# Kernel optimization log

Hardware: AMD Instinct MI355X
Metric: run time of the kernel (lower is better)

The kernel has to match this reference:

```python
import jax, jax.numpy as jnp
from jax import lax
import numpy as np

B, H, W, C = 64, 224, 224, 3
OH, OW = 224, 224
EPS = 1e-3  # keras BatchNormalization default epsilon
FLAT = 52 * 52 * 10  # after conv7(valid)->pool2->conv5(valid)->pool2 on 224x224


def setup_inputs() -> dict:
    key = jax.random.key(0)
    ks = jax.random.split(key, 6)
    return {
        "x": jax.random.normal(ks[0], (B, H, W, C), jnp.float32),
        "c1_w": jax.random.normal(ks[1], (7, 7, C, 8), jnp.float32) * 0.05,
        "c1_b": jnp.zeros((8,), jnp.float32),
        "g1": jnp.ones((8,), jnp.float32),
        "b1": jnp.zeros((8,), jnp.float32),
        "m1": jnp.zeros((8,), jnp.float32),
        "v1": jnp.ones((8,), jnp.float32),
        "c2_w": jax.random.normal(ks[2], (5, 5, 8, 10), jnp.float32) * 0.05,
        "c2_b": jnp.zeros((10,), jnp.float32),
        "g2": jnp.ones((10,), jnp.float32),
        "b2": jnp.zeros((10,), jnp.float32),
        "m2": jnp.zeros((10,), jnp.float32),
        "v2": jnp.ones((10,), jnp.float32),
        "d1_w": jax.random.normal(ks[3], (FLAT, 32), jnp.float32) * 0.01,
        "d1_b": jnp.zeros((32,), jnp.float32),
        "d2_w": jax.random.normal(ks[4], (32, 6), jnp.float32) * 0.01,
        "d2_b": jnp.array([1.0, 0.0, 0.0, 0.0, 1.0, 0.0], jnp.float32),  # identity affine
    }


def _conv(x, w, b):
    return lax.conv_general_dilated(x, w, (1, 1), 'VALID',
                                    dimension_numbers=('NHWC', 'HWIO', 'NHWC')) + b


def _maxpool(x):
    return lax.reduce_window(x, -jnp.inf, lax.max, (1, 2, 2, 1), (1, 2, 2, 1), 'VALID')


def _bn(x, g, b, m, v):
    # inference-mode batchnorm: gamma*(x-mean)/sqrt(var+eps)+beta
    return (x - m) * lax.rsqrt(v + EPS) * g + b


def _bilinear(img, px, py):
    # img: [H,W,C]; px,py: [OH,OW] pixel-space sample coords; zero fill outside
    x0 = jnp.floor(px).astype(jnp.int32)
    y0 = jnp.floor(py).astype(jnp.int32)

    def gather(yi, xi):
        valid = (yi >= 0) & (yi < H) & (xi >= 0) & (xi < W)
        v = img[jnp.clip(yi, 0, H - 1), jnp.clip(xi, 0, W - 1)]  # [OH,OW,C]
        return v * valid[..., None]

    wx = (px - x0)[..., None]
    wy = (py - y0)[..., None]
    return (gather(y0, x0) * (1 - wx) * (1 - wy)
            + gather(y0, x0 + 1) * wx * (1 - wy)
            + gather(y0 + 1, x0) * (1 - wx) * wy
            + gather(y0 + 1, x0 + 1) * wx * wy)


def reference(x, c1_w, c1_b, g1, b1, m1, v1, c2_w, c2_b, g2, b2, m2, v2,
              d1_w, d1_b, d2_w, d2_b):
    # localization network
    h = _maxpool(_bn(jax.nn.relu(_conv(x, c1_w, c1_b)), g1, b1, m1, v1))
    h = _maxpool(_bn(jax.nn.relu(_conv(h, c2_w, c2_b)), g2, b2, m2, v2))
    h = h.reshape(h.shape[0], -1)                      # [B, FLAT]
    h = jax.nn.relu(h @ d1_w + d1_b)                   # [B, 32]
    theta = (h @ d2_w + d2_b).reshape(-1, 2, 3)        # [B, 2, 3]

    # normalized homogeneous grid [N,3] with N = OH*OW
    xs = jnp.linspace(-1.0, 1.0, OW)
    ys = jnp.linspace(-1.0, 1.0, OH)
    xg, yg = jnp.meshgrid(xs, ys)
    grid = jnp.stack([xg.ravel(), yg.ravel(), jnp.ones(OH * OW, jnp.float32)], axis=-1)

    coords = jnp.einsum('bij,nj->bni', theta, grid)    # [B, N, 2]
    px = ((coords[..., 0] + 1.0) * 0.5 * (W - 1)).reshape(-1, OH, OW)
    py = ((coords[..., 1] + 1.0) * 0.5 * (H - 1)).reshape(-1, OH, OW)
    return jax.vmap(_bilinear)(x, px, py)              # [B, OH, OW, C]
```

## Files before the change

### kernel.cpp

```cpp
#include <hip/hip_runtime.h>
#include <hip/hip_bf16.h>


#define NCHUNK 212
#define KC 128

__global__ __launch_bounds__(256) void k_conv1(
    const float* __restrict__ x, const float* __restrict__ w,
    const float* __restrict__ bias, const float* __restrict__ g,
    const float* __restrict__ bt, const float* __restrict__ m,
    const float* __restrict__ v, float* __restrict__ out) {
  __shared__ float s_in[3][38][40];
  __shared__ float s_scale[8], s_shift[8], s_bias[8];
  const int tid = threadIdx.x;
  const int bx = blockIdx.x, by = blockIdx.y, b = blockIdx.z;

  if (tid < 8) {
    float sc = g[tid] * rsqrtf(v[tid] + 1e-3f);
    s_scale[tid] = sc;
    s_shift[tid] = bt[tid] - m[tid] * sc;
    s_bias[tid] = bias[tid];
  }
  const int iy0 = by * 32, ix0 = bx * 32;
  const float* xb = x + (size_t)b * 224 * 224 * 3;
  for (int f = tid; f < 38 * 114; f += 256) {
    int r = f / 114, rem = f - r * 114;
    int q = rem / 3, c = rem - q * 3;
    int gy = iy0 + r; if (gy > 223) gy = 223;
    int gc = ix0 + q; if (gc > 223) gc = 223;
    s_in[c][r][q] = xb[(gy * 224 + gc) * 3 + c];
  }
  __syncthreads();

  const int pyl = tid >> 4, pxl = tid & 15;
  const int ly = 2 * pyl, lx = 2 * pxl;
  float acc[4][8];
#pragma unroll
  for (int i = 0; i < 4; i++)
#pragma unroll
    for (int j = 0; j < 8; j++) acc[i][j] = 0.f;

#pragma unroll 1
  for (int r = 0; r < 8; ++r) {
    float row[3][8];
#pragma unroll
    for (int ci = 0; ci < 3; ci++)
#pragma unroll
      for (int j = 0; j < 4; j++) {
        float2 t = *(const float2*)&s_in[ci][ly + r][lx + 2 * j];
        row[ci][2 * j] = t.x; row[ci][2 * j + 1] = t.y;
      }
    if (r < 7) {
#pragma unroll
      for (int kx = 0; kx < 7; kx++)
#pragma unroll
        for (int ci = 0; ci < 3; ci++) {
          const float* wp = &w[((r * 7 + kx) * 3 + ci) * 8];
          float i0 = row[ci][kx], i1 = row[ci][kx + 1];
#pragma unroll
          for (int co = 0; co < 8; co++) {
            float wv = wp[co];
            acc[0][co] = fmaf(i0, wv, acc[0][co]);
            acc[1][co] = fmaf(i1, wv, acc[1][co]);
          }
        }
    }
    if (r >= 1) {
#pragma unroll
      for (int kx = 0; kx < 7; kx++)
#pragma unroll
        for (int ci = 0; ci < 3; ci++) {
          const float* wp = &w[(((r - 1) * 7 + kx) * 3 + ci) * 8];
          float i0 = row[ci][kx], i1 = row[ci][kx + 1];
#pragma unroll
          for (int co = 0; co < 8; co++) {
            float wv = wp[co];
            acc[2][co] = fmaf(i0, wv, acc[2][co]);
            acc[3][co] = fmaf(i1, wv, acc[3][co]);
          }
        }
    }
  }

  const int py = by * 16 + pyl, px = bx * 16 + pxl;
  if (py < 109 && px < 109) {
#pragma unroll
    for (int co = 0; co < 8; co++) {
      float sc = s_scale[co], sh = s_shift[co], bs = s_bias[co];
      float a0 = fmaxf(acc[0][co] + bs, 0.f) * sc + sh;
      float a1 = fmaxf(acc[1][co] + bs, 0.f) * sc + sh;
      float a2 = fmaxf(acc[2][co] + bs, 0.f) * sc + sh;
      float a3 = fmaxf(acc[3][co] + bs, 0.f) * sc + sh;
      out[(((size_t)co * 64 + b) * 109 + py) * 109 + px] =
          fmaxf(fmaxf(a0, a1), fmaxf(a2, a3));
    }
  }
}

__global__ __launch_bounds__(256) void k_conv2(
    const float* __restrict__ in, const float* __restrict__ w,
    const float* __restrict__ bias, const float* __restrict__ g,
    const float* __restrict__ bt, const float* __restrict__ m,
    const float* __restrict__ v, float* __restrict__ out) {
  __shared__ float s_in[8][36][40];
  __shared__ float s_scale[10], s_shift[10], s_bias[10];
  const int tid = threadIdx.x;
  const int bx = blockIdx.x, by = blockIdx.y, b = blockIdx.z;

  if (tid < 10) {
    float sc = g[tid] * rsqrtf(v[tid] + 1e-3f);
    s_scale[tid] = sc;
    s_shift[tid] = bt[tid] - m[tid] * sc;
    s_bias[tid] = bias[tid];
  }
  const int iy0 = by * 32, ix0 = bx * 32;
  for (int f = tid; f < 8 * 36 * 36; f += 256) {
    int ci = f / 1296, rem = f - ci * 1296;
    int r = rem / 36, q = rem - r * 36;
    int gy = iy0 + r; if (gy > 108) gy = 108;
    int gc = ix0 + q; if (gc > 108) gc = 108;
    s_in[ci][r][q] = in[(((size_t)ci * 64 + b) * 109 + gy) * 109 + gc];
  }
  __syncthreads();

  const int pyl = tid >> 4, pxl = tid & 15;
  const int ly = 2 * pyl, lx = 2 * pxl;
  float acc[4][10];
#pragma unroll
  for (int i = 0; i < 4; i++)
#pragma unroll
    for (int j = 0; j < 10; j++) acc[i][j] = 0.f;

#pragma unroll 1
  for (int r = 0; r < 6; ++r) {
    float row[8][6];
#pragma unroll
    for (int ci = 0; ci < 8; ci++)
#pragma unroll
      for (int j = 0; j < 3; j++) {
        float2 t = *(const float2*)&s_in[ci][ly + r][lx + 2 * j];
        row[ci][2 * j] = t.x; row[ci][2 * j + 1] = t.y;
      }
    if (r < 5) {
#pragma unroll
      for (int kx = 0; kx < 5; kx++)
#pragma unroll
        for (int ci = 0; ci < 8; ci++) {
          const float* wp = &w[((r * 5 + kx) * 8 + ci) * 10];
          float i0 = row[ci][kx], i1 = row[ci][kx + 1];
#pragma unroll
          for (int co = 0; co < 10; co++) {
            float wv = wp[co];
            acc[0][co] = fmaf(i0, wv, acc[0][co]);
            acc[1][co] = fmaf(i1, wv, acc[1][co]);
          }
        }
    }
    if (r >= 1) {
#pragma unroll
      for (int kx = 0; kx < 5; kx++)
#pragma unroll
        for (int ci = 0; ci < 8; ci++) {
          const float* wp = &w[(((r - 1) * 5 + kx) * 8 + ci) * 10];
          float i0 = row[ci][kx], i1 = row[ci][kx + 1];
#pragma unroll
          for (int co = 0; co < 10; co++) {
            float wv = wp[co];
            acc[2][co] = fmaf(i0, wv, acc[2][co]);
            acc[3][co] = fmaf(i1, wv, acc[3][co]);
          }
        }
    }
  }

  const int py = by * 16 + pyl, px = bx * 16 + pxl;
  if (py < 52 && px < 52) {
    float res[10];
#pragma unroll
    for (int co = 0; co < 10; co++) {
      float sc = s_scale[co], sh = s_shift[co], bs = s_bias[co];
      float a0 = fmaxf(acc[0][co] + bs, 0.f) * sc + sh;
      float a1 = fmaxf(acc[1][co] + bs, 0.f) * sc + sh;
      float a2 = fmaxf(acc[2][co] + bs, 0.f) * sc + sh;
      float a3 = fmaxf(acc[3][co] + bs, 0.f) * sc + sh;
      res[co] = fmaxf(fmaxf(a0, a1), fmaxf(a2, a3));
    }
    float2* op2 = (float2*)&out[(((size_t)b * 52 + py) * 52 + px) * 10];
#pragma unroll
    for (int i = 0; i < 5; i++)
      op2[i] = make_float2(res[2 * i], res[2 * i + 1]);
  }
}

__global__ __launch_bounds__(256) void k_fc1(
    const float* __restrict__ act, const float* __restrict__ w,
    float* __restrict__ partial) {
  __shared__ float s_w[KC * 32];
  __shared__ float s_a[64 * KC];
  const int tid = threadIdx.x;
  const int chunk = blockIdx.x;
  const int k0 = chunk * KC;
  for (int f = tid; f < KC * 32; f += 256) {
    int k = k0 + (f >> 5);
    s_w[f] = (k < 27040) ? w[(size_t)k0 * 32 + f] : 0.f;
  }
  for (int f = tid; f < 64 * KC; f += 256) {
    int bb = f >> 7, j = f & (KC - 1);
    int k = k0 + j;
    s_a[f] = (k < 27040) ? act[(size_t)bb * 27040 + k] : 0.f;
  }
  __syncthreads();
  const int o = tid & 31, bh = tid >> 5;
  float sums[8];
#pragma unroll
  for (int i = 0; i < 8; i++) sums[i] = 0.f;
#pragma unroll 1
  for (int j = 0; j < KC; j++) {
    float wv = s_w[j * 32 + o];
#pragma unroll
    for (int i = 0; i < 8; i++)
      sums[i] = fmaf(s_a[(i * 8 + bh) * KC + j], wv, sums[i]);
  }
#pragma unroll
  for (int i = 0; i < 8; i++)
    partial[(size_t)chunk * 2048 + i * 256 + tid] = sums[i];
}

__global__ __launch_bounds__(64) void k_fc2(
    const float* __restrict__ partial, const float* __restrict__ d1b,
    const float* __restrict__ d2w, const float* __restrict__ d2b,
    float* __restrict__ theta) {
  const int b = blockIdx.x;
  const int t = threadIdx.x;
  const int o = t & 31, half = t >> 5;
  float s = 0.f;
  const int c0 = half * (NCHUNK / 2), c1 = c0 + (NCHUNK / 2);
  for (int c = c0; c < c1; c++)
    s += partial[(size_t)c * 2048 + b * 32 + o];
  s += __shfl_down(s, 32);
  __shared__ float s_h[32];
  if (t < 32) s_h[o] = fmaxf(s + d1b[o], 0.f);
  __syncthreads();
  if (t < 6) {
    float th = d2b[t];
#pragma unroll
    for (int o2 = 0; o2 < 32; o2++) th = fmaf(s_h[o2], d2w[o2 * 6 + t], th);
    theta[b * 6 + t] = th;
  }
}

__global__ __launch_bounds__(256) void k_sample(
    const float* __restrict__ x, const float* __restrict__ theta,
    float* __restrict__ out) {
  const int b = blockIdx.y;
  __shared__ float th[6];
  if (threadIdx.x < 6) th[threadIdx.x] = theta[b * 6 + threadIdx.x];
  __syncthreads();
  const int t = blockIdx.x * 256 + threadIdx.x;
  const int oy = t / 224, ox = t - oy * 224;
  const float xn = -1.f + (2.f / 223.f) * (float)ox;
  const float yn = -1.f + (2.f / 223.f) * (float)oy;
  const float cx = th[0] * xn + th[1] * yn + th[2];
  const float cy = th[3] * xn + th[4] * yn + th[5];
  const float px = (cx + 1.f) * 0.5f * 223.f;
  const float py = (cy + 1.f) * 0.5f * 223.f;
  const float x0f = floorf(px), y0f = floorf(py);
  const int x0 = (int)x0f, y0 = (int)y0f;
  const float wx = px - x0f, wy = py - y0f;
  const float* xb = x + (size_t)b * 224 * 224 * 3;
  float a0 = 0.f, a1 = 0.f, a2 = 0.f;
#pragma unroll
  for (int dy = 0; dy < 2; dy++) {
    const int yi = y0 + dy;
    const bool vy = (yi >= 0) && (yi < 224);
    const int yc = yi < 0 ? 0 : (yi > 223 ? 223 : yi);
    const float wyv = dy ? wy : 1.f - wy;
#pragma unroll
    for (int dx = 0; dx < 2; dx++) {
      const int xi = x0 + dx;
      const bool vx = (xi >= 0) && (xi < 224);
      const int xc = xi < 0 ? 0 : (xi > 223 ? 223 : xi);
      const float wv = wyv * (dx ? wx : 1.f - wx) * ((vx && vy) ? 1.f : 0.f);
      const float* p = &xb[(yc * 224 + xc) * 3];
      a0 = fmaf(p[0], wv, a0);
      a1 = fmaf(p[1], wv, a1);
      a2 = fmaf(p[2], wv, a2);
    }
  }
  float* op = &out[((size_t)b * 50176 + t) * 3];
  op[0] = a0; op[1] = a1; op[2] = a2;
}

extern "C" void kernel_launch(void* const* d_in, const int* in_sizes, int n_in,
                              void* d_out, int out_size, void* d_ws, size_t ws_size,
                              hipStream_t stream) {
  const float* x    = (const float*)d_in[0];
  const float* c1w  = (const float*)d_in[1];
  const float* c1b  = (const float*)d_in[2];
  const float* g1   = (const float*)d_in[3];
  const float* b1   = (const float*)d_in[4];
  const float* m1   = (const float*)d_in[5];
  const float* v1   = (const float*)d_in[6];
  const float* c2w  = (const float*)d_in[7];
  const float* c2b  = (const float*)d_in[8];
  const float* g2   = (const float*)d_in[9];
  const float* b2   = (const float*)d_in[10];
  const float* m2   = (const float*)d_in[11];
  const float* v2   = (const float*)d_in[12];
  const float* d1w  = (const float*)d_in[13];
  const float* d1b  = (const float*)d_in[14];
  const float* d2w  = (const float*)d_in[15];
  const float* d2b  = (const float*)d_in[16];
  float* out = (float*)d_out;

  float* ws = (float*)d_ws;
  float* p1    = ws;
  float* p2    = p1 + 6083072;
  float* part  = p2 + 1730560;
  float* theta = part + (size_t)NCHUNK * 2048;

  k_conv1<<<dim3(7, 7, 64), 256, 0, stream>>>(x, c1w, c1b, g1, b1, m1, v1, p1);
  k_conv2<<<dim3(4, 4, 64), 256, 0, stream>>>(p1, c2w, c2b, g2, b2, m2, v2, p2);
  k_fc1<<<NCHUNK, 256, 0, stream>>>(p2, d1w, part);
  k_fc2<<<64, 64, 0, stream>>>(part, d1b, d2w, d2b, theta);
  k_sample<<<dim3(196, 64), 256, 0, stream>>>(x, theta, out);
}
```

Baseline: 316.9 us.

## Register-block conv kernels 4x4 per thread, stage weights in LDS, halve FC chunks

Both convolution kernels switch from 256 threads computing a 2x2 pre-pool patch each to 64 threads computing a 4x4 pre-pool patch (four pooled outputs) each. This raises register reuse of input rows and weights per FMA. conv1 stages its weights in shared memory and reads them as float4, and conv2 loads its input channels in two phases of four to shrink shared memory. The intermediate conv1 buffer gets a padded row stride of 110 so stores can be float2. The FC1 chunk size is halved to double the block count, and the partial buffer now reuses the workspace at p1. The larger per-thread accumulator arrays risk heavy register pressure and low occupancy with only one wave per block.

New measurement: 376.4 us. 1.19x slower.

```diff
diff --git a/kernel.cpp b/kernel.cpp
--- a/kernel.cpp
+++ b/kernel.cpp
@@ -2,19 +2,21 @@
 #include <hip/hip_bf16.h>
 
 
-#define NCHUNK 212
-#define KC 128
-
-__global__ __launch_bounds__(256) void k_conv1(
+#define NCHUNK 424
+#define KC 64
+
+__global__ __launch_bounds__(64) void k_conv1(
     const float* __restrict__ x, const float* __restrict__ w,
     const float* __restrict__ bias, const float* __restrict__ g,
     const float* __restrict__ bt, const float* __restrict__ m,
     const float* __restrict__ v, float* __restrict__ out) {
-  __shared__ float s_in[3][38][40];
+  __shared__ float s_in[3][38][42];
+  __shared__ float s_w[1176];
   __shared__ float s_scale[8], s_shift[8], s_bias[8];
   const int tid = threadIdx.x;
   const int bx = blockIdx.x, by = blockIdx.y, b = blockIdx.z;
 
+  for (int f = tid; f < 1176; f += 64) s_w[f] = w[f];
   if (tid < 8) {
     float sc = g[tid] * rsqrtf(v[tid] + 1e-3f);
     s_scale[tid] = sc;
@@ -23,7 +25,7 @@
   }
   const int iy0 = by * 32, ix0 = bx * 32;
   const float* xb = x + (size_t)b * 224 * 224 * 3;
-  for (int f = tid; f < 38 * 114; f += 256) {
+  for (int f = tid; f < 38 * 114; f += 64) {
     int r = f / 114, rem = f - r * 114;
     int q = rem / 3, c = rem - q * 3;
     int gy = iy0 + r; if (gy > 223) gy = 223;
@@ -32,77 +34,82 @@
   }
   __syncthreads();
 
-  const int pyl = tid >> 4, pxl = tid & 15;
-  const int ly = 2 * pyl, lx = 2 * pxl;
-  float acc[4][8];
+  const int tx = tid & 7, ty = tid >> 3;
+  const int ly = 4 * ty, lx = 4 * tx;
+  float acc[4][4][8];
 #pragma unroll
   for (int i = 0; i < 4; i++)
 #pragma unroll
-    for (int j = 0; j < 8; j++) acc[i][j] = 0.f;
-
-#pragma unroll 1
-  for (int r = 0; r < 8; ++r) {
-    float row[3][8];
-#pragma unroll
-    for (int ci = 0; ci < 3; ci++)
-#pragma unroll
-      for (int j = 0; j < 4; j++) {
-        float2 t = *(const float2*)&s_in[ci][ly + r][lx + 2 * j];
-        row[ci][2 * j] = t.x; row[ci][2 * j + 1] = t.y;
-      }
-    if (r < 7) {
-#pragma unroll
-      for (int kx = 0; kx < 7; kx++)
-#pragma unroll
-        for (int ci = 0; ci < 3; ci++) {
-          const float* wp = &w[((r * 7 + kx) * 3 + ci) * 8];
-          float i0 = row[ci][kx], i1 = row[ci][kx + 1];
-#pragma unroll
-          for (int co = 0; co < 8; co++) {
-            float wv = wp[co];
-            acc[0][co] = fmaf(i0, wv, acc[0][co]);
-            acc[1][co] = fmaf(i1, wv, acc[1][co]);
+    for (int j = 0; j < 4; j++)
+#pragma unroll
+      for (int k = 0; k < 8; k++) acc[i][j][k] = 0.f;
+
+#pragma unroll 1
+  for (int ky = 0; ky < 7; ++ky) {
+#pragma unroll 1
+    for (int ci = 0; ci < 3; ++ci) {
+      float rows[4][10];
+#pragma unroll
+      for (int rr = 0; rr < 4; ++rr)
+#pragma unroll
+        for (int j = 0; j < 5; ++j) {
+          float2 t = *(const float2*)&s_in[ci][ly + ky + rr][lx + 2 * j];
+          rows[rr][2 * j] = t.x; rows[rr][2 * j + 1] = t.y;
+        }
+      const int wbase = ky * 168 + ci * 8;
+#pragma unroll
+      for (int kx = 0; kx < 7; ++kx) {
+        float4 w0 = *(const float4*)&s_w[wbase + kx * 24];
+        float4 w1 = *(const float4*)&s_w[wbase + kx * 24 + 4];
+        float wv[8] = {w0.x, w0.y, w0.z, w0.w, w1.x, w1.y, w1.z, w1.w};
+#pragma unroll
+        for (int rr = 0; rr < 4; ++rr)
+#pragma unroll
+          for (int cc = 0; cc < 4; ++cc) {
+            float iv = rows[rr][cc + kx];
+#pragma unroll
+            for (int co = 0; co < 8; ++co)
+              acc[rr][cc][co] = fmaf(iv, wv[co], acc[rr][cc][co]);
           }
-        }
-    }
-    if (r >= 1) {
-#pragma unroll
-      for (int kx = 0; kx < 7; kx++)
-#pragma unroll
-        for (int ci = 0; ci < 3; ci++) {
-          const float* wp = &w[(((r - 1) * 7 + kx) * 3 + ci) * 8];
-          float i0 = row[ci][kx], i1 = row[ci][kx + 1];
-#pragma unroll
-          for (int co = 0; co < 8; co++) {
-            float wv = wp[co];
-            acc[2][co] = fmaf(i0, wv, acc[2][co]);
-            acc[3][co] = fmaf(i1, wv, acc[3][co]);
-          }
-        }
-    }
-  }
-
-  const int py = by * 16 + pyl, px = bx * 16 + pxl;
-  if (py < 109 && px < 109) {
-#pragma unroll
-    for (int co = 0; co < 8; co++) {
-      float sc = s_scale[co], sh = s_shift[co], bs = s_bias[co];
-      float a0 = fmaxf(acc[0][co] + bs, 0.f) * sc + sh;
-      float a1 = fmaxf(acc[1][co] + bs, 0.f) * sc + sh;
-      float a2 = fmaxf(acc[2][co] + bs, 0.f) * sc + sh;
-      float a3 = fmaxf(acc[3][co] + bs, 0.f) * sc + sh;
-      out[(((size_t)co * 64 + b) * 109 + py) * 109 + px] =
-          fmaxf(fmaxf(a0, a1), fmaxf(a2, a3));
-    }
-  }
-}
-
-__global__ __launch_bounds__(256) void k_conv2(
+      }
+    }
+  }
+
+  const int pby = by * 16 + 2 * ty, pbx = bx * 16 + 2 * tx;
+#pragma unroll
+  for (int co = 0; co < 8; ++co) {
+    float sc = s_scale[co], sh = s_shift[co], bs = s_bias[co];
+    float pv[2][2];
+#pragma unroll
+    for (int pr = 0; pr < 2; ++pr)
+#pragma unroll
+      for (int pc = 0; pc < 2; ++pc) {
+        float a0 = fmaxf(acc[2 * pr][2 * pc][co] + bs, 0.f) * sc + sh;
+        float a1 = fmaxf(acc[2 * pr][2 * pc + 1][co] + bs, 0.f) * sc + sh;
+        float a2 = fmaxf(acc[2 * pr + 1][2 * pc][co] + bs, 0.f) * sc + sh;
+        float a3 = fmaxf(acc[2 * pr + 1][2 * pc + 1][co] + bs, 0.f) * sc + sh;
+        pv[pr][pc] = fmaxf(fmaxf(a0, a1), fmaxf(a2, a3));
+      }
+    float* plane = out + ((size_t)co * 64 + b) * 109 * 110;
+#pragma unroll
+    for (int pr = 0; pr < 2; ++pr) {
+      int py = pby + pr;
+      if (py < 109) {
+        if (pbx + 1 < 109)
+          *(float2*)&plane[py * 110 + pbx] = make_float2(pv[pr][0], pv[pr][1]);
+        else if (pbx < 109)
+          plane[py * 110 + pbx] = pv[pr][0];
+      }
+    }
+  }
+}
+
+__global__ __launch_bounds__(64) void k_conv2(
     const float* __restrict__ in, const float* __restrict__ w,
     const float* __restrict__ bias, const float* __restrict__ g,
     const float* __restrict__ bt, const float* __restrict__ m,
     const float* __restrict__ v, float* __restrict__ out) {
-  __shared__ float s_in[8][36][40];
+  __shared__ float s_in[4][36][42];
   __shared__ float s_scale[10], s_shift[10], s_bias[10];
   const int tid = threadIdx.x;
   const int bx = blockIdx.x, by = blockIdx.y, b = blockIdx.z;
@@ -114,81 +121,88 @@
     s_bias[tid] = bias[tid];
   }
   const int iy0 = by * 32, ix0 = bx * 32;
-  for (int f = tid; f < 8 * 36 * 36; f += 256) {
-    int ci = f / 1296, rem = f - ci * 1296;
-    int r = rem / 36, q = rem - r * 36;
-    int gy = iy0 + r; if (gy > 108) gy = 108;
-    int gc = ix0 + q; if (gc > 108) gc = 108;
-    s_in[ci][r][q] = in[(((size_t)ci * 64 + b) * 109 + gy) * 109 + gc];
-  }
-  __syncthreads();
-
-  const int pyl = tid >> 4, pxl = tid & 15;
-  const int ly = 2 * pyl, lx = 2 * pxl;
-  float acc[4][10];
+  const int tx = tid & 7, ty = tid >> 3;
+  const int ly = 4 * ty, lx = 4 * tx;
+  float acc[4][4][10];
 #pragma unroll
   for (int i = 0; i < 4; i++)
 #pragma unroll
-    for (int j = 0; j < 10; j++) acc[i][j] = 0.f;
-
-#pragma unroll 1
-  for (int r = 0; r < 6; ++r) {
-    float row[8][6];
-#pragma unroll
-    for (int ci = 0; ci < 8; ci++)
-#pragma unroll
-      for (int j = 0; j < 3; j++) {
-        float2 t = *(const float2*)&s_in[ci][ly + r][lx + 2 * j];
-        row[ci][2 * j] = t.x; row[ci][2 * j + 1] = t.y;
-      }
-    if (r < 5) {
-#pragma unroll
-      for (int kx = 0; kx < 5; kx++)
-#pragma unroll
-        for (int ci = 0; ci < 8; ci++) {
-          const float* wp = &w[((r * 5 + kx) * 8 + ci) * 10];
-          float i0 = row[ci][kx], i1 = row[ci][kx + 1];
-#pragma unroll
-          for (int co = 0; co < 10; co++) {
-            float wv = wp[co];
-            acc[0][co] = fmaf(i0, wv, acc[0][co]);
-            acc[1][co] = fmaf(i1, wv, acc[1][co]);
+    for (int j = 0; j < 4; j++)
+#pragma unroll
+      for (int k = 0; k < 10; k++) acc[i][j][k] = 0.f;
+
+#pragma unroll 1
+  for (int ph = 0; ph < 2; ++ph) {
+    __syncthreads();
+    for (int f = tid; f < 4 * 36 * 36; f += 64) {
+      int ci = f / 1296, rem = f - ci * 1296;
+      int r = rem / 36, q = rem - r * 36;
+      int gy = iy0 + r; if (gy > 108) gy = 108;
+      int gc = ix0 + q; if (gc > 108) gc = 108;
+      s_in[ci][r][q] = in[(((size_t)(ph * 4 + ci) * 64 + b) * 109 + gy) * 110 + gc];
+    }
+    __syncthreads();
+
+#pragma unroll 1
+    for (int ky = 0; ky < 5; ++ky) {
+#pragma unroll 1
+      for (int ci = 0; ci < 4; ++ci) {
+        float rows[4][8];
+#pragma unroll
+        for (int rr = 0; rr < 4; ++rr)
+#pragma unroll
+          for (int j = 0; j < 4; ++j) {
+            float2 t = *(const float2*)&s_in[ci][ly + ky + rr][lx + 2 * j];
+            rows[rr][2 * j] = t.x; rows[rr][2 * j + 1] = t.y;
           }
+        const float* wrow = w + (ky * 5) * 80 + (ph * 4 + ci) * 10;
+#pragma unroll
+        for (int kx = 0; kx < 5; ++kx) {
+          const float* wp = wrow + kx * 80;
+          float wv[10];
+#pragma unroll
+          for (int u = 0; u < 5; ++u) {
+            float2 t = *(const float2*)&wp[2 * u];
+            wv[2 * u] = t.x; wv[2 * u + 1] = t.y;
+          }
+#pragma unroll
+          for (int rr = 0; rr < 4; ++rr)
+#pragma unroll
+            for (int cc = 0; cc < 4; ++cc) {
+              float iv = rows[rr][cc + kx];
+#pragma unroll
+              for (int co = 0; co < 10; ++co)
+                acc[rr][cc][co] = fmaf(iv, wv[co], acc[rr][cc][co]);
+            }
         }
-    }
-    if (r >= 1) {
-#pragma unroll
-      for (int kx = 0; kx < 5; kx++)
-#pragma unroll
-        for (int ci = 0; ci < 8; ci++) {
-          const float* wp = &w[(((r - 1) * 5 + kx) * 8 + ci) * 10];
-          float i0 = row[ci][kx], i1 = row[ci][kx + 1];
-#pragma unroll
-          for (int co = 0; co < 10; co++) {
-            float wv = wp[co];
-            acc[2][co] = fmaf(i0, wv, acc[2][co]);
-            acc[3][co] = fmaf(i1, wv, acc[3][co]);
-          }
-        }
-    }
-  }
-
-  const int py = by * 16 + pyl, px = bx * 16 + pxl;
-  if (py < 52 && px < 52) {
-    float res[10];
-#pragma unroll
-    for (int co = 0; co < 10; co++) {
-      float sc = s_scale[co], sh = s_shift[co], bs = s_bias[co];
-      float a0 = fmaxf(acc[0][co] + bs, 0.f) * sc + sh;
-      float a1 = fmaxf(acc[1][co] + bs, 0.f) * sc + sh;
-      float a2 = fmaxf(acc[2][co] + bs, 0.f) * sc + sh;
-      float a3 = fmaxf(acc[3][co] + bs, 0.f) * sc + sh;
-      res[co] = fmaxf(fmaxf(a0, a1), fmaxf(a2, a3));
-    }
-    float2* op2 = (float2*)&out[(((size_t)b * 52 + py) * 52 + px) * 10];
-#pragma unroll
-    for (int i = 0; i < 5; i++)
-      op2[i] = make_float2(res[2 * i], res[2 * i + 1]);
+      }
+    }
+  }
+
+  const int pby = by * 16 + 2 * ty, pbx = bx * 16 + 2 * tx;
+#pragma unroll
+  for (int pr = 0; pr < 2; ++pr) {
+    int py = pby + pr;
+    if (py >= 52) continue;
+#pragma unroll
+    for (int pc = 0; pc < 2; ++pc) {
+      int px = pbx + pc;
+      if (px >= 52) continue;
+      float res[10];
+#pragma unroll
+      for (int co = 0; co < 10; ++co) {
+        float sc = s_scale[co], sh = s_shift[co], bs = s_bias[co];
+        float a0 = fmaxf(acc[2 * pr][2 * pc][co] + bs, 0.f) * sc + sh;
+        float a1 = fmaxf(acc[2 * pr][2 * pc + 1][co] + bs, 0.f) * sc + sh;
+        float a2 = fmaxf(acc[2 * pr + 1][2 * pc][co] + bs, 0.f) * sc + sh;
+        float a3 = fmaxf(acc[2 * pr + 1][2 * pc + 1][co] + bs, 0.f) * sc + sh;
+        res[co] = fmaxf(fmaxf(a0, a1), fmaxf(a2, a3));
+      }
+      float2* op2 = (float2*)&out[(((size_t)b * 52 + py) * 52 + px) * 10];
+#pragma unroll
+      for (int i = 0; i < 5; i++)
+        op2[i] = make_float2(res[2 * i], res[2 * i + 1]);
+    }
   }
 }
 
@@ -205,7 +219,7 @@
     s_w[f] = (k < 27040) ? w[(size_t)k0 * 32 + f] : 0.f;
   }
   for (int f = tid; f < 64 * KC; f += 256) {
-    int bb = f >> 7, j = f & (KC - 1);
+    int bb = f >> 6, j = f & (KC - 1);
     int k = k0 + j;
     s_a[f] = (k < 27040) ? act[(size_t)bb * 27040 + k] : 0.f;
   }
@@ -235,6 +249,7 @@
   const int o = t & 31, half = t >> 5;
   float s = 0.f;
   const int c0 = half * (NCHUNK / 2), c1 = c0 + (NCHUNK / 2);
+#pragma unroll 4
   for (int c = c0; c < c1; c++)
     s += partial[(size_t)c * 2048 + b * 32 + o];
   s += __shfl_down(s, 32);
@@ -315,12 +330,12 @@
 
   float* ws = (float*)d_ws;
   float* p1    = ws;
-  float* p2    = p1 + 6083072;
-  float* part  = p2 + 1730560;
-  float* theta = part + (size_t)NCHUNK * 2048;
-
-  k_conv1<<<dim3(7, 7, 64), 256, 0, stream>>>(x, c1w, c1b, g1, b1, m1, v1, p1);
-  k_conv2<<<dim3(4, 4, 64), 256, 0, stream>>>(p1, c2w, c2b, g2, b2, m2, v2, p2);
+  float* p2    = p1 + 6138880;
+  float* theta = p2 + 1730560;
+  float* part  = ws;
+
+  k_conv1<<<dim3(7, 7, 64), 64, 0, stream>>>(x, c1w, c1b, g1, b1, m1, v1, p1);
+  k_conv2<<<dim3(4, 4, 64), 64, 0, stream>>>(p1, c2w, c2b, g2, b2, m2, v2, p2);
   k_fc1<<<NCHUNK, 256, 0, stream>>>(p2, d1w, part);
   k_fc2<<<64, 64, 0, stream>>>(part, d1b, d2w, d2b, theta);
   k_sample<<<dim3(196, 64), 256, 0, stream>>>(x, theta, out);
```

## Restructure conv loops by input channel with register-cached weight rows

Applied to the files above, without the earlier changes.

Both convolution kernels now loop over input channels on the outside, load the whole input patch for that channel into registers, and per kernel row load a register block of weights with vector loads that feeds a 2x2 pooled output tile. This targets redundant scalar weight loads and the split accumulation branches of the old row loop. The shared-memory row pitch changes, the conv1 output row stride is padded to 110, and the fc partial buffer now aliases the p1 workspace. The reduction loop in fc2 is unrolled. Register pressure rises because of the larger register tiles, which may reduce occupancy.

Result: faster. 295.4 us (-6.8%).

```diff
diff --git a/kernel.cpp b/kernel.cpp
--- a/kernel.cpp
+++ b/kernel.cpp
@@ -10,16 +10,16 @@
     const float* __restrict__ bias, const float* __restrict__ g,
     const float* __restrict__ bt, const float* __restrict__ m,
     const float* __restrict__ v, float* __restrict__ out) {
-  __shared__ float s_in[3][38][40];
-  __shared__ float s_scale[8], s_shift[8], s_bias[8];
+  __shared__ float s_in[3][38][42];
+  __shared__ float s_bn[3][8];
   const int tid = threadIdx.x;
   const int bx = blockIdx.x, by = blockIdx.y, b = blockIdx.z;
 
   if (tid < 8) {
     float sc = g[tid] * rsqrtf(v[tid] + 1e-3f);
-    s_scale[tid] = sc;
-    s_shift[tid] = bt[tid] - m[tid] * sc;
-    s_bias[tid] = bias[tid];
+    s_bn[0][tid] = sc;
+    s_bn[1][tid] = bt[tid] - m[tid] * sc;
+    s_bn[2][tid] = bias[tid];
   }
   const int iy0 = by * 32, ix0 = bx * 32;
   const float* xb = x + (size_t)b * 224 * 224 * 3;
@@ -32,66 +32,61 @@
   }
   __syncthreads();
 
-  const int pyl = tid >> 4, pxl = tid & 15;
-  const int ly = 2 * pyl, lx = 2 * pxl;
-  float acc[4][8];
-#pragma unroll
-  for (int i = 0; i < 4; i++)
-#pragma unroll
-    for (int j = 0; j < 8; j++) acc[i][j] = 0.f;
+  const int pxl = tid & 15, pyl = tid >> 4;
+  const int lx = 2 * pxl, ly = 2 * pyl;
+  float acc[2][2][8];
+#pragma unroll
+  for (int pr = 0; pr < 2; ++pr)
+#pragma unroll
+    for (int pc = 0; pc < 2; ++pc)
+#pragma unroll
+      for (int co = 0; co < 8; ++co) acc[pr][pc][co] = 0.f;
 
 #pragma unroll 1
-  for (int r = 0; r < 8; ++r) {
-    float row[3][8];
-#pragma unroll
-    for (int ci = 0; ci < 3; ci++)
-#pragma unroll
-      for (int j = 0; j < 4; j++) {
+  for (int ci = 0; ci < 3; ++ci) {
+    float rw[8][8];
+#pragma unroll
+    for (int r = 0; r < 8; ++r)
+#pragma unroll
+      for (int j = 0; j < 4; ++j) {
         float2 t = *(const float2*)&s_in[ci][ly + r][lx + 2 * j];
-        row[ci][2 * j] = t.x; row[ci][2 * j + 1] = t.y;
+        rw[r][2 * j] = t.x; rw[r][2 * j + 1] = t.y;
       }
-    if (r < 7) {
-#pragma unroll
-      for (int kx = 0; kx < 7; kx++)
-#pragma unroll
-        for (int ci = 0; ci < 3; ci++) {
-          const float* wp = &w[((r * 7 + kx) * 3 + ci) * 8];
-          float i0 = row[ci][kx], i1 = row[ci][kx + 1];
-#pragma unroll
-          for (int co = 0; co < 8; co++) {
-            float wv = wp[co];
-            acc[0][co] = fmaf(i0, wv, acc[0][co]);
-            acc[1][co] = fmaf(i1, wv, acc[1][co]);
+#pragma unroll
+    for (int ky = 0; ky < 7; ++ky) {
+      float wv[7][8];
+#pragma unroll
+      for (int kx = 0; kx < 7; ++kx) {
+        const float* wp = w + ((ky * 7 + kx) * 3 + ci) * 8;
+        float4 a = *(const float4*)wp;
+        float4 c4 = *(const float4*)(wp + 4);
+        wv[kx][0] = a.x;  wv[kx][1] = a.y;  wv[kx][2] = a.z;  wv[kx][3] = a.w;
+        wv[kx][4] = c4.x; wv[kx][5] = c4.y; wv[kx][6] = c4.z; wv[kx][7] = c4.w;
+      }
+#pragma unroll
+      for (int kx = 0; kx < 7; ++kx)
+#pragma unroll
+        for (int pr = 0; pr < 2; ++pr)
+#pragma unroll
+          for (int pc = 0; pc < 2; ++pc) {
+            float iv = rw[ky + pr][kx + pc];
+#pragma unroll
+            for (int co = 0; co < 8; ++co)
+              acc[pr][pc][co] = fmaf(iv, wv[kx][co], acc[pr][pc][co]);
           }
-        }
-    }
-    if (r >= 1) {
-#pragma unroll
-      for (int kx = 0; kx < 7; kx++)
-#pragma unroll
-        for (int ci = 0; ci < 3; ci++) {
-          const float* wp = &w[(((r - 1) * 7 + kx) * 3 + ci) * 8];
-          float i0 = row[ci][kx], i1 = row[ci][kx + 1];
-#pragma unroll
-          for (int co = 0; co < 8; co++) {
-            float wv = wp[co];
-            acc[2][co] = fmaf(i0, wv, acc[2][co]);
-            acc[3][co] = fmaf(i1, wv, acc[3][co]);
-          }
-        }
     }
   }
 
   const int py = by * 16 + pyl, px = bx * 16 + pxl;
   if (py < 109 && px < 109) {
 #pragma unroll
-    for (int co = 0; co < 8; co++) {
-      float sc = s_scale[co], sh = s_shift[co], bs = s_bias[co];
-      float a0 = fmaxf(acc[0][co] + bs, 0.f) * sc + sh;
-      float a1 = fmaxf(acc[1][co] + bs, 0.f) * sc + sh;
-      float a2 = fmaxf(acc[2][co] + bs, 0.f) * sc + sh;
-      float a3 = fmaxf(acc[3][co] + bs, 0.f) * sc + sh;
-      out[(((size_t)co * 64 + b) * 109 + py) * 109 + px] =
+    for (int co = 0; co < 8; ++co) {
+      float sc = s_bn[0][co], sh = s_bn[1][co], bs = s_bn[2][co];
+      float a0 = fmaxf(acc[0][0][co] + bs, 0.f) * sc + sh;
+      float a1 = fmaxf(acc[0][1][co] + bs, 0.f) * sc + sh;
+      float a2 = fmaxf(acc[1][0][co] + bs, 0.f) * sc + sh;
+      float a3 = fmaxf(acc[1][1][co] + bs, 0.f) * sc + sh;
+      out[((size_t)co * 64 + b) * 109 * 110 + py * 110 + px] =
           fmaxf(fmaxf(a0, a1), fmaxf(a2, a3));
     }
   }
@@ -102,16 +97,16 @@
     const float* __restrict__ bias, const float* __restrict__ g,
     const float* __restrict__ bt, const float* __restrict__ m,
     const float* __restrict__ v, float* __restrict__ out) {
-  __shared__ float s_in[8][36][40];
-  __shared__ float s_scale[10], s_shift[10], s_bias[10];
+  __shared__ float s_in[8][36][38];
+  __shared__ float s_bn[3][10];
   const int tid = threadIdx.x;
   const int bx = blockIdx.x, by = blockIdx.y, b = blockIdx.z;
 
   if (tid < 10) {
     float sc = g[tid] * rsqrtf(v[tid] + 1e-3f);
-    s_scale[tid] = sc;
-    s_shift[tid] = bt[tid] - m[tid] * sc;
-    s_bias[tid] = bias[tid];
+    s_bn[0][tid] = sc;
+    s_bn[1][tid] = bt[tid] - m[tid] * sc;
+    s_bn[2][tid] = bias[tid];
   }
   const int iy0 = by * 32, ix0 = bx * 32;
   for (int f = tid; f < 8 * 36 * 36; f += 256) {
@@ -119,57 +114,53 @@
     int r = rem / 36, q = rem - r * 36;
     int gy = iy0 + r; if (gy > 108) gy = 108;
     int gc = ix0 + q; if (gc > 108) gc = 108;
-    s_in[ci][r][q] = in[(((size_t)ci * 64 + b) * 109 + gy) * 109 + gc];
-  }
-  __syncthreads();
-
-  const int pyl = tid >> 4, pxl = tid & 15;
-  const int ly = 2 * pyl, lx = 2 * pxl;
-  float acc[4][10];
-#pragma unroll
-  for (int i = 0; i < 4; i++)
-#pragma unroll
-    for (int j = 0; j < 10; j++) acc[i][j] = 0.f;
+    s_in[ci][r][q] = in[(((size_t)ci * 64 + b) * 109 + gy) * 110 + gc];
+  }
+  __syncthreads();
+
+  const int pxl = tid & 15, pyl = tid >> 4;
+  const int lx = 2 * pxl, ly = 2 * pyl;
+  float acc[2][2][10];
+#pragma unroll
+  for (int pr = 0; pr < 2; ++pr)
+#pragma unroll
+    for (int pc = 0; pc < 2; ++pc)
+#pragma unroll
+      for (int co = 0; co < 10; ++co) acc[pr][pc][co] = 0.f;
 
 #pragma unroll 1
-  for (int r = 0; r < 6; ++r) {
-    float row[8][6];
-#pragma unroll
-    for (int ci = 0; ci < 8; ci++)
-#pragma unroll
-      for (int j = 0; j < 3; j++) {
+  for (int ci = 0; ci < 8; ++ci) {
+    float rw[6][8];
+#pragma unroll
+    for (int r = 0; r < 6; ++r)
+#pragma unroll
+      for (int j = 0; j < 4; ++j) {
         float2 t = *(const float2*)&s_in[ci][ly + r][lx + 2 * j];
-        row[ci][2 * j] = t.x; row[ci][2 * j + 1] = t.y;
+        rw[r][2 * j] = t.x; rw[r][2 * j + 1] = t.y;
       }
-    if (r < 5) {
-#pragma unroll
-      for (int kx = 0; kx < 5; kx++)
-#pragma unroll
-        for (int ci = 0; ci < 8; ci++) {
-          const float* wp = &w[((r * 5 + kx) * 8 + ci) * 10];
-          float i0 = row[ci][kx], i1 = row[ci][kx + 1];
-#pragma unroll
-          for (int co = 0; co < 10; co++) {
-            float wv = wp[co];
-            acc[0][co] = fmaf(i0, wv, acc[0][co]);
-            acc[1][co] = fmaf(i1, wv, acc[1][co]);
+#pragma unroll
+    for (int ky = 0; ky < 5; ++ky) {
+      float wv[5][10];
+#pragma unroll
+      for (int kx = 0; kx < 5; ++kx) {
+        const float* wp = w + ((ky * 5 + kx) * 8 + ci) * 10;
+#pragma unroll
+        for (int u = 0; u < 5; ++u) {
+          float2 t = *(const float2*)(wp + 2 * u);
+          wv[kx][2 * u] = t.x; wv[kx][2 * u + 1] = t.y;
+        }
+      }
+#pragma unroll
+      for (int kx = 0; kx < 5; ++kx)
+#pragma unroll
+        for (int pr = 0; pr < 2; ++pr)
+#pragma unroll
+          for (int pc = 0; pc < 2; ++pc) {
+            float iv = rw[ky + pr][kx + pc];
+#pragma unroll
+            for (int co = 0; co < 10; ++co)
+              acc[pr][pc][co] = fmaf(iv, wv[kx][co], acc[pr][pc][co]);
           }
-        }
-    }
-    if (r >= 1) {
-#pragma unroll
-      for (int kx = 0; kx < 5; kx++)
-#pragma unroll
-        for (int ci = 0; ci < 8; ci++) {
-          const float* wp = &w[(((r - 1) * 5 + kx) * 8 + ci) * 10];
-          float i0 = row[ci][kx], i1 = row[ci][kx + 1];
-#pragma unroll
-          for (int co = 0; co < 10; co++) {
-            float wv = wp[co];
-            acc[2][co] = fmaf(i0, wv, acc[2][co]);
-            acc[3][co] = fmaf(i1, wv, acc[3][co]);
-          }
-        }
     }
   }
 
@@ -177,12 +168,12 @@
   if (py < 52 && px < 52) {
     float res[10];
 #pragma unroll
-    for (int co = 0; co < 10; co++) {
-      float sc = s_scale[co], sh = s_shift[co], bs = s_bias[co];
-      float a0 = fmaxf(acc[0][co] + bs, 0.f) * sc + sh;
-      float a1 = fmaxf(acc[1][co] + bs, 0.f) * sc + sh;
-      float a2 = fmaxf(acc[2][co] + bs, 0.f) * sc + sh;
-      float a3 = fmaxf(acc[3][co] + bs, 0.f) * sc + sh;
+    for (int co = 0; co < 10; ++co) {
+      float sc = s_bn[0][co], sh = s_bn[1][co], bs = s_bn[2][co];
+      float a0 = fmaxf(acc[0][0][co] + bs, 0.f) * sc + sh;
+      float a1 = fmaxf(acc[0][1][co] + bs, 0.f) * sc + sh;
+      float a2 = fmaxf(acc[1][0][co] + bs, 0.f) * sc + sh;
+      float a3 = fmaxf(acc[1][1][co] + bs, 0.f) * sc + sh;
       res[co] = fmaxf(fmaxf(a0, a1), fmaxf(a2, a3));
     }
     float2* op2 = (float2*)&out[(((size_t)b * 52 + py) * 52 + px) * 10];
@@ -235,6 +226,7 @@
   const int o = t & 31, half = t >> 5;
   float s = 0.f;
   const int c0 = half * (NCHUNK / 2), c1 = c0 + (NCHUNK / 2);
+#pragma unroll 4
   for (int c = c0; c < c1; c++)
     s += partial[(size_t)c * 2048 + b * 32 + o];
   s += __shfl_down(s, 32);
@@ -315,9 +307,9 @@
 
   float* ws = (float*)d_ws;
   float* p1    = ws;
-  float* p2    = p1 + 6083072;
-  float* part  = p2 + 1730560;
-  float* theta = part + (size_t)NCHUNK * 2048;
+  float* p2    = p1 + 6138880;
+  float* theta = p2 + 1730560;
+  float* part  = ws;
 
   k_conv1<<<dim3(7, 7, 64), 256, 0, stream>>>(x, c1w, c1b, g1, b1, m1, v1, p1);
   k_conv2<<<dim3(4, 4, 64), 256, 0, stream>>>(p1, c2w, c2b, g2, b2, m2, v2, p2);
```
